# Kernel tuning notes

Measured on AMD Instinct MI355X. Metric: run time of the kernel, lower is better.

## Reference

```python
import jax, jax.numpy as jnp
import numpy as np

N = 8192
TOKEN_DIM = 384
K = 16
D_IN = 2 * (TOKEN_DIM + 3)  # 774


def setup_inputs() -> dict:
    key = jax.random.key(0)
    k1, k2, k3, k4, k5, k6 = jax.random.split(key, 6)
    xyz = jax.random.normal(k1, (N, 3), dtype=jnp.float32)
    feat = jax.random.normal(k2, (N, TOKEN_DIM), dtype=jnp.float32)
    W1 = jax.random.normal(k3, (D_IN, TOKEN_DIM), dtype=jnp.float32) / np.sqrt(D_IN)
    b1 = jax.random.normal(k4, (TOKEN_DIM,), dtype=jnp.float32) * 0.01
    W2 = jax.random.normal(k5, (TOKEN_DIM, 3), dtype=jnp.float32) / np.sqrt(TOKEN_DIM)
    b2 = jax.random.normal(k6, (3,), dtype=jnp.float32) * 0.01
    return {"xyz": xyz, "feat": feat, "W1": W1, "b1": b1, "W2": W2, "b2": b2}


def _knn_idx(xyz, k):
    # pairwise squared distances [N, N]; loop=False -> exclude self via +inf diag
    sq = jnp.sum(xyz * xyz, axis=-1)
    d2 = sq[:, None] + sq[None, :] - 2.0 * (xyz @ xyz.T)
    n = xyz.shape[0]
    d2 = jnp.where(jnp.eye(n, dtype=bool), jnp.inf, d2)
    _, idx = jax.lax.top_k(-d2, k)  # idx[i] = k nearest neighbors (sources) of target i
    return idx


def reference(xyz, feat, W1, b1, W2, b2):
    idx = _knn_idx(xyz, K)                      # [N, K] int32
    x = jnp.concatenate([feat, xyz], axis=-1)   # [N, D] with D = token_dim + 3
    x_j = x[idx]                                # [N, K, D] gathered neighbor feats
    x_i = x[:, None, :]                         # [N, 1, D]
    # EdgeConv message: nn(cat([x_i, x_j - x_i]))
    e = jnp.concatenate([jnp.broadcast_to(x_i, x_j.shape), x_j - x_i], axis=-1)  # [N, K, 2D]
    h = jax.nn.relu(jnp.einsum('nkd,df->nkf', e, W1) + b1)   # [N, K, token_dim]
    m = jnp.einsum('nkf,fo->nko', h, W2) + b2                # [N, K, 3]
    agg = jnp.max(m, axis=1)                                 # max aggregation over neighbors
    return xyz + agg
```

## Files before the change

### kernel.cpp

```cpp
#include <hip/hip_runtime.h>
#include <hip/hip_bf16.h>


#define N 8192
#define TD 384
#define KNN 16
#define DX 387
#define KP 416
#define NF 768
#define INFF __builtin_inff()

typedef __attribute__((ext_vector_type(8))) short short8;
typedef __attribute__((ext_vector_type(4))) float f32x4;
typedef __attribute__((ext_vector_type(2))) float f32x2;


__device__ __forceinline__ f32x2 pk_mul(f32x2 a, f32x2 b) {
    f32x2 r; asm("v_pk_mul_f32 %0, %1, %2" : "=v"(r) : "v"(a), "v"(b)); return r;
}
__device__ __forceinline__ f32x2 pk_add(f32x2 a, f32x2 b) {
    f32x2 r; asm("v_pk_add_f32 %0, %1, %2" : "=v"(r) : "v"(a), "v"(b)); return r;
}
__device__ __forceinline__ f32x2 pk_sub(f32x2 a, f32x2 b) {
    f32x2 r; asm("v_pk_add_f32 %0, %1, %2 neg_lo:[0,1] neg_hi:[0,1]" : "=v"(r) : "v"(a), "v"(b)); return r;
}
__device__ __forceinline__ f32x2 pk_fma(f32x2 a, f32x2 b, f32x2 c) {
    f32x2 r; asm("v_pk_fma_f32 %0, %1, %2, %3" : "=v"(r) : "v"(a), "v"(b), "v"(c)); return r;
}

__device__ __forceinline__ void dist4(f32x2 qx, f32x2 qy, f32x2 qz, f32x2 qw,
                                      f32x2 x01, f32x2 x23, f32x2 y01, f32x2 y23,
                                      f32x2 z01, f32x2 z23, f32x2 s01, f32x2 s23,
                                      f32x2& d01, f32x2& d23) {
    f32x2 dot01 = pk_fma(qz, z01, pk_fma(qy, y01, pk_mul(qx, x01)));
    f32x2 dot23 = pk_fma(qz, z23, pk_fma(qy, y23, pk_mul(qx, x23)));
    d01 = pk_sub(pk_add(qw, s01), pk_add(dot01, dot01));
    d23 = pk_sub(pk_add(qw, s23), pk_add(dot23, dot23));
}

__device__ __forceinline__ int xbin(float x) {
    int b = (int)((x + 4.0f) * 32.0f);
    return b < 0 ? 0 : (b > 255 ? 255 : b);
}


__global__ void __launch_bounds__(128) prep_all(const float* __restrict__ feat,
                                                const float* __restrict__ xyz,
                                                const float* __restrict__ W1,
                                                __hip_bfloat16* __restrict__ Xb,
                                                __hip_bfloat16* __restrict__ Wpt,
                                                int* __restrict__ cut) {
    int b = blockIdx.x;
    int t = threadIdx.x;
    if (b < N) {
        if (t < 96) {
            float4 f = reinterpret_cast<const float4*>(feat + (size_t)b*TD)[t];
            __hip_bfloat16 h[4] = {__float2bfloat16(f.x), __float2bfloat16(f.y),
                                   __float2bfloat16(f.z), __float2bfloat16(f.w)};
            *reinterpret_cast<ulonglong1*>(Xb + b*KP + t*4) = *reinterpret_cast<ulonglong1*>(h);
        } else if (t == 96) {
            for (int d = TD; d < KP; ++d) {
                float v = (d < DX) ? xyz[b*3 + (d - TD)] : 0.f;
                Xb[b*KP + d] = __float2bfloat16(v);
            }
        }
    } else if (b < N + NF) {
        int f = b - N;
        for (int k = t; k < KP; k += 128) {
            float v = 0.f;
            if (k < DX) {
                if (f < TD) v = W1[k*TD + f] - W1[(DX+k)*TD + f];
                else        v = W1[(DX+k)*TD + (f - TD)];
            }
            Wpt[f*KP + k] = __float2bfloat16(v);
        }
    } else {
        cut[t] = 0;
        cut[t + 128] = 0;
    }
}


__global__ void __launch_bounds__(256) assign_kernel(const float* __restrict__ xyz,
                                                     int* __restrict__ cut,
                                                     int* __restrict__ tlo,
                                                     int* __restrict__ thi,
                                                     float* __restrict__ stile) {
    __shared__ int hcnt[256];
    __shared__ int base[256];
    __shared__ int stlo[32], sthi[32];
    const int t = threadIdx.x;

    hcnt[t] = 0;
    if (t < 32) { stlo[t] = 255; sthi[t] = 0; }
    __syncthreads();

    #pragma unroll
    for (int c = 0; c < 32; ++c) {
        atomicAdd(&hcnt[xbin(xyz[(t + c*256)*3])], 1);
    }
    __syncthreads();

    const int v = hcnt[t];
    base[t] = v;
    __syncthreads();
    for (int off = 1; off < 256; off <<= 1) {
        int add = (t >= off) ? base[t - off] : 0;
        __syncthreads();
        base[t] += add;
        __syncthreads();
    }
    const int end = base[t], start = end - v;
    __syncthreads();
    base[t] = start;
    __syncthreads();

    if (blockIdx.x == 0) {
        if (v > 0) {
            for (int x = start >> 8; x <= (end - 1) >> 8; ++x) {
                atomicMin(&stlo[x], t);
                atomicMax(&sthi[x], t);
            }
        }
        __syncthreads();
        if (t < 32) { tlo[t] = stlo[t]; thi[t] = sthi[t]; }
    }

    const int i = blockIdx.x * 256 + t;
    float x = xyz[i*3+0], y = xyz[i*3+1], z = xyz[i*3+2];
    int bin = xbin(x);
    int pos = base[bin] + atomicAdd(&cut[bin], 1);
    float sq = __fadd_rn(__fadd_rn(__fmul_rn(x,x), __fmul_rn(y,y)), __fmul_rn(z,z));
    float* tp = stile + (pos >> 8) * 1280 + (pos & 255);
    tp[0] = x; tp[256] = y; tp[512] = z; tp[768] = sq;
    reinterpret_cast<int*>(tp)[1024] = i;
}


__device__ __forceinline__ float rdlane_f(float v, int src) {
    return __uint_as_float(__builtin_amdgcn_readlane(__float_as_uint(v), src));
}
__device__ __forceinline__ unsigned udmap(float x) {
    unsigned u = __float_as_uint(x);
    return ((int)u < 0) ? ~u : (u | 0x80000000u);
}


__global__ void __launch_bounds__(256, 8) knn_kernel(const float* __restrict__ stile,
                                                     const int* __restrict__ tlo,
                                                     const int* __restrict__ thi,
                                                     int* __restrict__ knn) {
    __shared__ unsigned sbuf[4][128][2];
    const int lane = threadIdx.x & 63;
    const int wv   = threadIdx.x >> 6;
    const int s    = blockIdx.x * 4 + wv;
    const int tq   = s >> 8;
    const int sl   = (s & 255) >> 2;
    const int slot = s & 3;

    const float* qp = stile + tq*1280 + (s & 255);
    const float qx = qp[0], qy = qp[256], qz = qp[512], qw = qp[768];
    const int   qi = reinterpret_cast<const int*>(qp)[1024];
    const f32x2 qx2 = {qx,qx}, qy2 = {qy,qy}, qz2 = {qz,qz}, qw2 = {qw,qw};

    const float* lbase = stile + lane*4;
    const bool is_self_lane = (lane == sl);

    float mn = INFF;
    int lo = tq - 2; if (lo < 0) lo = 0; if (lo > 27) lo = 27;
    #pragma unroll
    for (int tt = 0; tt < 5; ++tt) {
        const int t = lo + tt;
        const float* tp = lbase + t*1280;
        float4 X = *(const float4*)(tp);
        float4 Y = *(const float4*)(tp + 256);
        float4 Z = *(const float4*)(tp + 512);
        float4 S = *(const float4*)(tp + 768);
        f32x2 x01 = {X.x,X.y}, x23 = {X.z,X.w};
        f32x2 y01 = {Y.x,Y.y}, y23 = {Y.z,Y.w};
        f32x2 z01 = {Z.x,Z.y}, z23 = {Z.z,Z.w};
        f32x2 s01 = {S.x,S.y}, s23 = {S.z,S.w};
        f32x2 d01, d23;
        dist4(qx2, qy2, qz2, qw2, x01, x23, y01, y23, z01, z23, s01, s23, d01, d23);
        if ((t == tq) && is_self_lane) {
            if      (slot == 0) d01[0] = INFF;
            else if (slot == 1) d01[1] = INFF;
            else if (slot == 2) d23[0] = INFF;
            else                d23[1] = INFF;
        }
        mn = fminf(mn, fminf(fminf(d01[0], d01[1]), fminf(d23[0], d23[1])));
    }

    float T;
    {
        unsigned ub = udmap(mn);
        unsigned long long alive = ~0ull;
        int need = KNN;
        #pragma unroll
        for (int b = 31; b >= 0; --b) {
            unsigned long long ones  = __ballot(((ub >> b) & 1u) != 0u);
            unsigned long long zeros = alive & ~ones;
            int cz = (int)__popcll(zeros);
            bool tz = (cz >= need);
            alive = tz ? zeros : (alive & ones);
            need  = tz ? need : (need - cz);
        }
        T = fmaxf(rdlane_f(mn, (int)__ffsll(alive) - 1), 0.f);
    }

    unsigned mask;
    {
        const int ti = lane & 31;
        const int bl = tlo[ti], bh = thi[ti];
        const float xlo = (bl == 0)   ? -1e30f : (bl * 0.03125f - 4.0f);
        const float xhi = (bh == 255) ?  1e30f : ((bh + 1) * 0.03125f - 4.0f);
        float gap = fmaxf(0.f, fmaxf(xlo - qx, qx - xhi));
        bool gate = (gap * gap <= T + 1e-3f);
        mask = (unsigned)__ballot(gate && (lane < 32));
    }

    int cnt = 0;
    const unsigned long long ltm = (1ull << lane) - 1;

    auto push = [&](float dv, int idx) {
        bool pred = (dv <= T);
        unsigned long long bal = __ballot(pred);
        if (bal) {
            int posn = cnt + (int)__popcll(bal & ltm);
            if (pred && posn < 128) {
                sbuf[wv][posn][0] = udmap(dv);
                sbuf[wv][posn][1] = (unsigned)idx;
            }
            cnt += (int)__popcll(bal);
        }
    };

    while (mask) {
        const int t = (int)__ffs(mask) - 1;
        mask &= mask - 1;
        const float* tp = lbase + t*1280;
        float4 X = *(const float4*)(tp);
        float4 Y = *(const float4*)(tp + 256);
        float4 Z = *(const float4*)(tp + 512);
        float4 S = *(const float4*)(tp + 768);
        int4   I = *(const int4*)(tp + 1024);
        f32x2 x01 = {X.x,X.y}, x23 = {X.z,X.w};
        f32x2 y01 = {Y.x,Y.y}, y23 = {Y.z,Y.w};
        f32x2 z01 = {Z.x,Z.y}, z23 = {Z.z,Z.w};
        f32x2 s01 = {S.x,S.y}, s23 = {S.z,S.w};
        f32x2 d01, d23;
        dist4(qx2, qy2, qz2, qw2, x01, x23, y01, y23, z01, z23, s01, s23, d01, d23);
        if ((t == tq) && is_self_lane) {
            if      (slot == 0) d01[0] = INFF;
            else if (slot == 1) d01[1] = INFF;
            else if (slot == 2) d23[0] = INFF;
            else                d23[1] = INFF;
        }
        float tmin = fminf(fminf(d01[0], d01[1]), fminf(d23[0], d23[1]));
        if (__ballot(tmin <= T)) {
            push(d01[0], I.x);
            push(d01[1], I.y);
            push(d23[0], I.z);
            push(d23[1], I.w);
        }
    }

    asm volatile("s_waitcnt lgkmcnt(0)" ::: "memory");
    const int M = (cnt > 128) ? 128 : cnt;
    unsigned ud1 = 0xFFFFFFFFu, id1 = 0xFFFFFFFFu;
    unsigned ud2 = 0xFFFFFFFFu, id2 = 0xFFFFFFFFu;
    if (lane < M)      { ud1 = sbuf[wv][lane][0];      id1 = sbuf[wv][lane][1]; }
    if (lane + 64 < M) { ud2 = sbuf[wv][lane + 64][0]; id2 = sbuf[wv][lane + 64][1]; }

    unsigned long long alive1 = __ballot(lane < M);
    unsigned long long alive2 = __ballot(lane + 64 < M);
    int need = KNN;
    #pragma unroll
    for (int b = 31; b >= 0; --b) {
        unsigned long long on1 = __ballot(((ud1 >> b) & 1u) != 0u);
        unsigned long long on2 = __ballot(((ud2 >> b) & 1u) != 0u);
        unsigned long long z1 = alive1 & ~on1;
        unsigned long long z2 = alive2 & ~on2;
        int cz = (int)__popcll(z1) + (int)__popcll(z2);
        bool tz = (cz >= need);
        alive1 = tz ? z1 : (alive1 & on1);
        alive2 = tz ? z2 : (alive2 & on2);
        need   = tz ? need : (need - cz);
    }
    unsigned v16;
    if (alive1) v16 = (unsigned)__builtin_amdgcn_readlane((int)ud1, (int)__ffsll(alive1) - 1);
    else        v16 = (unsigned)__builtin_amdgcn_readlane((int)ud2, (int)__ffsll(alive2) - 1);

    const int nt = (int)__popcll(alive1) + (int)__popcll(alive2);
    const bool all_ties = (nt <= need);
    unsigned vidx = 0xFFFFFFFFu;
    if (!all_ties) {
        unsigned long long a1 = alive1, a2 = alive2;
        int nd = need;
        for (int b = 31; b >= 0; --b) {
            unsigned long long on1 = __ballot(((id1 >> b) & 1u) != 0u);
            unsigned long long on2 = __ballot(((id2 >> b) & 1u) != 0u);
            unsigned long long z1 = a1 & ~on1;
            unsigned long long z2 = a2 & ~on2;
            int cz = (int)__popcll(z1) + (int)__popcll(z2);
            bool tz = (cz >= nd);
            a1 = tz ? z1 : (a1 & on1);
            a2 = tz ? z2 : (a2 & on2);
            nd = tz ? nd : (nd - cz);
        }
        if (a1) vidx = (unsigned)__builtin_amdgcn_readlane((int)id1, (int)__ffsll(a1) - 1);
        else    vidx = (unsigned)__builtin_amdgcn_readlane((int)id2, (int)__ffsll(a2) - 1);
    }

    bool sel1 = (lane < M)      && ((ud1 < v16) || ((ud1 == v16) && (all_ties || (id1 <= vidx))));
    bool sel2 = (lane + 64 < M) && ((ud2 < v16) || ((ud2 == v16) && (all_ties || (id2 <= vidx))));
    unsigned long long bs1 = __ballot(sel1);
    if (sel1) knn[qi*KNN + (int)__popcll(bs1 & ltm)] = (int)id1;
    const int c1 = (int)__popcll(bs1);
    unsigned long long bs2 = __ballot(sel2);
    if (sel2) knn[qi*KNN + c1 + (int)__popcll(bs2 & ltm)] = (int)id2;
}


__global__ void __launch_bounds__(64) gemm_kernel(const __hip_bfloat16* __restrict__ Xb,
                                                  const __hip_bfloat16* __restrict__ Wpt,
                                                  const float* __restrict__ b1,
                                                  __hip_bfloat16* __restrict__ Ub,
                                                  __hip_bfloat16* __restrict__ Vb) {
    const int lane = threadIdx.x;
    const int i0   = blockIdx.x * 64;
    const int f0   = blockIdx.y * 64;
    const int lm   = lane & 15;
    const int lk   = (lane >> 4) * 8;

    f32x4 acc[4][4];
    #pragma unroll
    for (int r = 0; r < 4; ++r)
        #pragma unroll
        for (int c = 0; c < 4; ++c)
            acc[r][c] = (f32x4){0.f, 0.f, 0.f, 0.f};

    const __hip_bfloat16* xbase = Xb  + (size_t)(i0 + lm) * KP + lk;
    const __hip_bfloat16* wbase = Wpt + (size_t)(f0 + lm) * KP + lk;

    #pragma unroll
    for (int kk = 0; kk < 13; ++kk) {
        short8 a[4], b[4];
        #pragma unroll
        for (int r = 0; r < 4; ++r)
            a[r] = *reinterpret_cast<const short8*>(xbase + (size_t)r*16*KP + kk*32);
        #pragma unroll
        for (int c = 0; c < 4; ++c)
            b[c] = *reinterpret_cast<const short8*>(wbase + (size_t)c*16*KP + kk*32);
        #pragma unroll
        for (int r = 0; r < 4; ++r)
            #pragma unroll
            for (int c = 0; c < 4; ++c)
                acc[r][c] = __builtin_amdgcn_mfma_f32_16x16x32_bf16(a[r], b[c], acc[r][c], 0, 0, 0);
    }

    const bool isU = (f0 < TD);
    __hip_bfloat16* outb = isU ? (Ub + f0) : (Vb + (f0 - TD));
    float bias[4] = {0.f, 0.f, 0.f, 0.f};
    if (isU) {
        #pragma unroll
        for (int c = 0; c < 4; ++c) bias[c] = b1[f0 + c*16 + lm];
    }
    const int crow = (lane >> 4) * 4;
    #pragma unroll
    for (int r = 0; r < 4; ++r)
        #pragma unroll
        for (int c = 0; c < 4; ++c)
            #pragma unroll
            for (int q = 0; q < 4; ++q)
                outb[(size_t)(i0 + r*16 + crow + q) * TD + c*16 + lm] =
                    __float2bfloat16(acc[r][c][q] + bias[c]);
}


__device__ __forceinline__ float bflo(unsigned w) { return __uint_as_float(w << 16); }
__device__ __forceinline__ float bfhi(unsigned w) { return __uint_as_float(w & 0xFFFF0000u); }

template<int CTRL>
__device__ __forceinline__ float dppf(float v) {
    return __uint_as_float((unsigned)__builtin_amdgcn_update_dpp(
        0, (int)__float_as_uint(v), CTRL, 0xF, 0xF, true));
}

__global__ void __launch_bounds__(256) final_kernel(const __hip_bfloat16* __restrict__ Ub,
                                                    const __hip_bfloat16* __restrict__ Vb,
                                                    const int* __restrict__ knn,
                                                    const float* __restrict__ xyz,
                                                    const float* __restrict__ W2,
                                                    const float* __restrict__ b2,
                                                    float* __restrict__ out) {
    const int lane = threadIdx.x & 63;
    const int wv   = threadIdx.x >> 6;
    const int i    = blockIdx.x * 4 + wv;
    const int d0   = lane * 6;

    int jreg = knn[i*KNN + (lane & 15)];

    float u[6], w2l[6][3];
    {
        const unsigned* rowU = reinterpret_cast<const unsigned*>(Ub + (size_t)i * TD) + lane*3;
        unsigned a0 = rowU[0], a1 = rowU[1], a2 = rowU[2];
        u[0] = bflo(a0); u[1] = bfhi(a0);
        u[2] = bflo(a1); u[3] = bfhi(a1);
        u[4] = bflo(a2); u[5] = bfhi(a2);
    }
    #pragma unroll
    for (int t = 0; t < 6; ++t)
        #pragma unroll
        for (int c = 0; c < 3; ++c) w2l[t][c] = W2[(d0 + t)*3 + c];

    const unsigned* vbase = reinterpret_cast<const unsigned*>(Vb);
    const int voff = lane * 3;

    float pk0[16], pk1[16], pk2[16];
    unsigned va[2][4][3];

    #pragma unroll
    for (int t = 0; t < 4; ++t) {
        int j = __builtin_amdgcn_readlane(jreg, t);
        const unsigned* rv = vbase + (size_t)j * 192 + voff;
        va[0][t][0] = rv[0]; va[0][t][1] = rv[1]; va[0][t][2] = rv[2];
    }
    __builtin_amdgcn_sched_barrier(0);

    #pragma unroll
    for (int b = 0; b < 4; ++b) {
        if (b < 3) {
            #pragma unroll
            for (int t = 0; t < 4; ++t) {
                int j = __builtin_amdgcn_readlane(jreg, (b+1)*4 + t);
                const unsigned* rv = vbase + (size_t)j * 192 + voff;
                va[(b+1)&1][t][0] = rv[0];
                va[(b+1)&1][t][1] = rv[1];
                va[(b+1)&1][t][2] = rv[2];
            }
            __builtin_amdgcn_sched_barrier(0);
        }
        #pragma unroll
        for (int t = 0; t < 4; ++t) {
            const int kk = b*4 + t;
            unsigned a0 = va[b&1][t][0], a1 = va[b&1][t][1], a2 = va[b&1][t][2];
            float v0 = bflo(a0), v1 = bfhi(a0);
            float v2 = bflo(a1), v3 = bfhi(a1);
            float v4 = bflo(a2), v5 = bfhi(a2);
            float h0 = fmaxf(u[0] + v0, 0.f), h1 = fmaxf(u[1] + v1, 0.f);
            float h2 = fmaxf(u[2] + v2, 0.f), h3 = fmaxf(u[3] + v3, 0.f);
            float h4 = fmaxf(u[4] + v4, 0.f), h5 = fmaxf(u[5] + v5, 0.f);
            float s0 = 0.f, s1 = 0.f, s2 = 0.f;
            s0 = fmaf(h0, w2l[0][0], s0); s1 = fmaf(h0, w2l[0][1], s1); s2 = fmaf(h0, w2l[0][2], s2);
            s0 = fmaf(h1, w2l[1][0], s0); s1 = fmaf(h1, w2l[1][1], s1); s2 = fmaf(h1, w2l[1][2], s2);
            s0 = fmaf(h2, w2l[2][0], s0); s1 = fmaf(h2, w2l[2][1], s1); s2 = fmaf(h2, w2l[2][2], s2);
            s0 = fmaf(h3, w2l[3][0], s0); s1 = fmaf(h3, w2l[3][1], s1); s2 = fmaf(h3, w2l[3][2], s2);
            s0 = fmaf(h4, w2l[4][0], s0); s1 = fmaf(h4, w2l[4][1], s1); s2 = fmaf(h4, w2l[4][2], s2);
            s0 = fmaf(h5, w2l[5][0], s0); s1 = fmaf(h5, w2l[5][1], s1); s2 = fmaf(h5, w2l[5][2], s2);
            pk0[kk] = s0; pk1[kk] = s1; pk2[kk] = s2;
        }
    }

    #pragma unroll
    for (int kk = 0; kk < 16; ++kk) {
        float r0 = pk0[kk], r1 = pk1[kk], r2 = pk2[kk];
        r0 += dppf<0x121>(r0); r1 += dppf<0x121>(r1); r2 += dppf<0x121>(r2);
        r0 += dppf<0x122>(r0); r1 += dppf<0x122>(r1); r2 += dppf<0x122>(r2);
        r0 += dppf<0x124>(r0); r1 += dppf<0x124>(r1); r2 += dppf<0x124>(r2);
        r0 += dppf<0x128>(r0); r1 += dppf<0x128>(r1); r2 += dppf<0x128>(r2);
        r0 += __shfl_xor(r0, 16); r1 += __shfl_xor(r1, 16); r2 += __shfl_xor(r2, 16);
        r0 += __shfl_xor(r0, 32); r1 += __shfl_xor(r1, 32); r2 += __shfl_xor(r2, 32);
        pk0[kk] = r0; pk1[kk] = r1; pk2[kk] = r2;
    }
    float mx0 = pk0[0], mx1 = pk1[0], mx2 = pk2[0];
    #pragma unroll
    for (int kk = 1; kk < 16; ++kk) {
        mx0 = fmaxf(mx0, pk0[kk]);
        mx1 = fmaxf(mx1, pk1[kk]);
        mx2 = fmaxf(mx2, pk2[kk]);
    }

    if (lane == 0) {
        out[i*3+0] = xyz[i*3+0] + mx0 + b2[0];
        out[i*3+1] = xyz[i*3+1] + mx1 + b2[1];
        out[i*3+2] = xyz[i*3+2] + mx2 + b2[2];
    }
}


extern "C" void kernel_launch(void* const* d_in, const int* in_sizes, int n_in,
                              void* d_out, int out_size, void* d_ws, size_t ws_size,
                              hipStream_t stream) {
    const float* xyz  = (const float*)d_in[0];
    const float* feat = (const float*)d_in[1];
    const float* W1   = (const float*)d_in[2];
    const float* b1   = (const float*)d_in[3];
    const float* W2   = (const float*)d_in[4];
    const float* b2   = (const float*)d_in[5];
    float* out = (float*)d_out;

    char* ws = (char*)d_ws;
    int*            knn   = (int*)(ws + 0);
    float*          stile = (float*)(ws + 524288);
    __hip_bfloat16* Xb    = (__hip_bfloat16*)(ws + 688128);
    __hip_bfloat16* Wpt   = (__hip_bfloat16*)(ws + 7503872);
    __hip_bfloat16* Ub    = (__hip_bfloat16*)(ws + 8142848);
    __hip_bfloat16* Vb    = (__hip_bfloat16*)(ws + 14434304);
    int*            cut   = (int*)(ws + 20725760);
    int*            thi   = (int*)(ws + 20726784);
    int*            tlo   = (int*)(ws + 20726912);

    prep_all     <<<dim3(N + NF + 1),  dim3(128), 0, stream>>>(feat, xyz, W1, Xb, Wpt, cut);
    assign_kernel<<<dim3(N/256),       dim3(256), 0, stream>>>(xyz, cut, tlo, thi, stile);
    knn_kernel   <<<dim3(N/4),         dim3(256), 0, stream>>>(stile, tlo, thi, knn);
    gemm_kernel  <<<dim3(N/64, NF/64), dim3(64),  0, stream>>>(Xb, Wpt, b1, Ub, Vb);
    final_kernel <<<dim3(N/4),         dim3(256), 0, stream>>>(Ub, Vb, knn, xyz, W2, b2, out);
}
```

Before: 85.96 us.

## Cache first-pass KNN distances in LDS and add single-wave fast select path

The KNN kernel now stores the distances computed for the first five tiles in shared memory and reuses them in the candidate-collection pass instead of reloading coordinates and recomputing. A specialised one-register selection path runs when there are at most 64 candidates, and the prep kernel now writes the xyz/pad columns in parallel across threads instead of in a one-thread loop. The extra LDS (20KB per block) lowers the occupancy hint from 8 to 6 waves, trading occupancy for less recompute and fewer global loads.

```diff
diff --git a/kernel.cpp b/kernel.cpp
--- a/kernel.cpp
+++ b/kernel.cpp
@@ -58,11 +58,10 @@
             __hip_bfloat16 h[4] = {__float2bfloat16(f.x), __float2bfloat16(f.y),
                                    __float2bfloat16(f.z), __float2bfloat16(f.w)};
             *reinterpret_cast<ulonglong1*>(Xb + b*KP + t*4) = *reinterpret_cast<ulonglong1*>(h);
-        } else if (t == 96) {
-            for (int d = TD; d < KP; ++d) {
-                float v = (d < DX) ? xyz[b*3 + (d - TD)] : 0.f;
-                Xb[b*KP + d] = __float2bfloat16(v);
-            }
+        } else {
+            int d = TD + (t - 96);
+            float v = (d < DX) ? xyz[b*3 + (d - TD)] : 0.f;
+            Xb[b*KP + d] = __float2bfloat16(v);
         }
     } else if (b < N + NF) {
         int f = b - N;
@@ -146,10 +145,11 @@
 }
 
 
-__global__ void __launch_bounds__(256, 8) knn_kernel(const float* __restrict__ stile,
+__global__ void __launch_bounds__(256, 6) knn_kernel(const float* __restrict__ stile,
                                                      const int* __restrict__ tlo,
                                                      const int* __restrict__ thi,
                                                      int* __restrict__ knn) {
+    __shared__ float    dcache[4][5][256];
     __shared__ unsigned sbuf[4][128][2];
     const int lane = threadIdx.x & 63;
     const int wv   = threadIdx.x >> 6;
@@ -188,7 +188,9 @@
             else if (slot == 2) d23[0] = INFF;
             else                d23[1] = INFF;
         }
-        mn = fminf(mn, fminf(fminf(d01[0], d01[1]), fminf(d23[0], d23[1])));
+        f32x4 dd = {d01[0], d01[1], d23[0], d23[1]};
+        *reinterpret_cast<f32x4*>(&dcache[wv][tt][lane*4]) = dd;
+        mn = fminf(mn, fminf(fminf(dd[0], dd[1]), fminf(dd[2], dd[3])));
     }
 
     float T;
@@ -235,9 +237,21 @@
         }
     };
 
-    while (mask) {
-        const int t = (int)__ffs(mask) - 1;
-        mask &= mask - 1;
+    #pragma unroll
+    for (int tt = 0; tt < 5; ++tt) {
+        const int t = lo + tt;
+        if (!((mask >> t) & 1u)) continue;
+        f32x4 dd = *reinterpret_cast<const f32x4*>(&dcache[wv][tt][lane*4]);
+        int4 I = *(const int4*)(lbase + t*1280 + 1024);
+        push(dd[0], I.x);
+        push(dd[1], I.y);
+        push(dd[2], I.z);
+        push(dd[3], I.w);
+    }
+    unsigned rest = mask & ~(0x1Fu << lo);
+    while (rest) {
+        const int t = (int)__ffs(rest) - 1;
+        rest &= rest - 1;
         const float* tp = lbase + t*1280;
         float4 X = *(const float4*)(tp);
         float4 Y = *(const float4*)(tp + 256);
@@ -250,12 +264,6 @@
         f32x2 s01 = {S.x,S.y}, s23 = {S.z,S.w};
         f32x2 d01, d23;
         dist4(qx2, qy2, qz2, qw2, x01, x23, y01, y23, z01, z23, s01, s23, d01, d23);
-        if ((t == tq) && is_self_lane) {
-            if      (slot == 0) d01[0] = INFF;
-            else if (slot == 1) d01[1] = INFF;
-            else if (slot == 2) d23[0] = INFF;
-            else                d23[1] = INFF;
-        }
         float tmin = fminf(fminf(d01[0], d01[1]), fminf(d23[0], d23[1]));
         if (__ballot(tmin <= T)) {
             push(d01[0], I.x);
@@ -267,58 +275,94 @@
 
     asm volatile("s_waitcnt lgkmcnt(0)" ::: "memory");
     const int M = (cnt > 128) ? 128 : cnt;
-    unsigned ud1 = 0xFFFFFFFFu, id1 = 0xFFFFFFFFu;
-    unsigned ud2 = 0xFFFFFFFFu, id2 = 0xFFFFFFFFu;
-    if (lane < M)      { ud1 = sbuf[wv][lane][0];      id1 = sbuf[wv][lane][1]; }
-    if (lane + 64 < M) { ud2 = sbuf[wv][lane + 64][0]; id2 = sbuf[wv][lane + 64][1]; }
-
-    unsigned long long alive1 = __ballot(lane < M);
-    unsigned long long alive2 = __ballot(lane + 64 < M);
-    int need = KNN;
-    #pragma unroll
-    for (int b = 31; b >= 0; --b) {
-        unsigned long long on1 = __ballot(((ud1 >> b) & 1u) != 0u);
-        unsigned long long on2 = __ballot(((ud2 >> b) & 1u) != 0u);
-        unsigned long long z1 = alive1 & ~on1;
-        unsigned long long z2 = alive2 & ~on2;
-        int cz = (int)__popcll(z1) + (int)__popcll(z2);
-        bool tz = (cz >= need);
-        alive1 = tz ? z1 : (alive1 & on1);
-        alive2 = tz ? z2 : (alive2 & on2);
-        need   = tz ? need : (need - cz);
-    }
-    unsigned v16;
-    if (alive1) v16 = (unsigned)__builtin_amdgcn_readlane((int)ud1, (int)__ffsll(alive1) - 1);
-    else        v16 = (unsigned)__builtin_amdgcn_readlane((int)ud2, (int)__ffsll(alive2) - 1);
-
-    const int nt = (int)__popcll(alive1) + (int)__popcll(alive2);
-    const bool all_ties = (nt <= need);
-    unsigned vidx = 0xFFFFFFFFu;
-    if (!all_ties) {
-        unsigned long long a1 = alive1, a2 = alive2;
-        int nd = need;
+
+    if (M <= 64) {
+        unsigned ud1 = 0xFFFFFFFFu, id1 = 0xFFFFFFFFu;
+        if (lane < M) { ud1 = sbuf[wv][lane][0]; id1 = sbuf[wv][lane][1]; }
+        unsigned long long alive = __ballot(lane < M);
+        int need = KNN;
+        #pragma unroll
         for (int b = 31; b >= 0; --b) {
-            unsigned long long on1 = __ballot(((id1 >> b) & 1u) != 0u);
-            unsigned long long on2 = __ballot(((id2 >> b) & 1u) != 0u);
-            unsigned long long z1 = a1 & ~on1;
-            unsigned long long z2 = a2 & ~on2;
+            unsigned long long on = __ballot(((ud1 >> b) & 1u) != 0u);
+            unsigned long long z  = alive & ~on;
+            int cz = (int)__popcll(z);
+            bool tz = (cz >= need);
+            alive = tz ? z : (alive & on);
+            need  = tz ? need : (need - cz);
+        }
+        unsigned v16 = (unsigned)__builtin_amdgcn_readlane((int)ud1, (int)__ffsll(alive) - 1);
+        const bool all_ties = ((int)__popcll(alive) <= need);
+        unsigned vidx = 0xFFFFFFFFu;
+        if (!all_ties) {
+            unsigned long long a = alive;
+            int nd = need;
+            for (int b = 31; b >= 0; --b) {
+                unsigned long long on = __ballot(((id1 >> b) & 1u) != 0u);
+                unsigned long long z  = a & ~on;
+                int cz = (int)__popcll(z);
+                bool tz = (cz >= nd);
+                a  = tz ? z : (a & on);
+                nd = tz ? nd : (nd - cz);
+            }
+            vidx = (unsigned)__builtin_amdgcn_readlane((int)id1, (int)__ffsll(a) - 1);
+        }
+        bool sel = (lane < M) && ((ud1 < v16) || ((ud1 == v16) && (all_ties || (id1 <= vidx))));
+        unsigned long long bs = __ballot(sel);
+        if (sel) knn[qi*KNN + (int)__popcll(bs & ltm)] = (int)id1;
+    } else {
+        unsigned ud1 = 0xFFFFFFFFu, id1 = 0xFFFFFFFFu;
+        unsigned ud2 = 0xFFFFFFFFu, id2 = 0xFFFFFFFFu;
+        if (lane < M)      { ud1 = sbuf[wv][lane][0];      id1 = sbuf[wv][lane][1]; }
+        if (lane + 64 < M) { ud2 = sbuf[wv][lane + 64][0]; id2 = sbuf[wv][lane + 64][1]; }
+
+        unsigned long long alive1 = __ballot(lane < M);
+        unsigned long long alive2 = __ballot(lane + 64 < M);
+        int need = KNN;
+        #pragma unroll
+        for (int b = 31; b >= 0; --b) {
+            unsigned long long on1 = __ballot(((ud1 >> b) & 1u) != 0u);
+            unsigned long long on2 = __ballot(((ud2 >> b) & 1u) != 0u);
+            unsigned long long z1 = alive1 & ~on1;
+            unsigned long long z2 = alive2 & ~on2;
             int cz = (int)__popcll(z1) + (int)__popcll(z2);
-            bool tz = (cz >= nd);
-            a1 = tz ? z1 : (a1 & on1);
-            a2 = tz ? z2 : (a2 & on2);
-            nd = tz ? nd : (nd - cz);
-        }
-        if (a1) vidx = (unsigned)__builtin_amdgcn_readlane((int)id1, (int)__ffsll(a1) - 1);
-        else    vidx = (unsigned)__builtin_amdgcn_readlane((int)id2, (int)__ffsll(a2) - 1);
-    }
-
-    bool sel1 = (lane < M)      && ((ud1 < v16) || ((ud1 == v16) && (all_ties || (id1 <= vidx))));
-    bool sel2 = (lane + 64 < M) && ((ud2 < v16) || ((ud2 == v16) && (all_ties || (id2 <= vidx))));
-    unsigned long long bs1 = __ballot(sel1);
-    if (sel1) knn[qi*KNN + (int)__popcll(bs1 & ltm)] = (int)id1;
-    const int c1 = (int)__popcll(bs1);
-    unsigned long long bs2 = __ballot(sel2);
-    if (sel2) knn[qi*KNN + c1 + (int)__popcll(bs2 & ltm)] = (int)id2;
+            bool tz = (cz >= need);
+            alive1 = tz ? z1 : (alive1 & on1);
+            alive2 = tz ? z2 : (alive2 & on2);
+            need   = tz ? need : (need - cz);
+        }
+        unsigned v16;
+        if (alive1) v16 = (unsigned)__builtin_amdgcn_readlane((int)ud1, (int)__ffsll(alive1) - 1);
+        else        v16 = (unsigned)__builtin_amdgcn_readlane((int)ud2, (int)__ffsll(alive2) - 1);
+
+        const int nt = (int)__popcll(alive1) + (int)__popcll(alive2);
+        const bool all_ties = (nt <= need);
+        unsigned vidx = 0xFFFFFFFFu;
+        if (!all_ties) {
+            unsigned long long a1 = alive1, a2 = alive2;
+            int nd = need;
+            for (int b = 31; b >= 0; --b) {
+                unsigned long long on1 = __ballot(((id1 >> b) & 1u) != 0u);
+                unsigned long long on2 = __ballot(((id2 >> b) & 1u) != 0u);
+                unsigned long long z1 = a1 & ~on1;
+                unsigned long long z2 = a2 & ~on2;
+                int cz = (int)__popcll(z1) + (int)__popcll(z2);
+                bool tz = (cz >= nd);
+                a1 = tz ? z1 : (a1 & on1);
+                a2 = tz ? z2 : (a2 & on2);
+                nd = tz ? nd : (nd - cz);
+            }
+            if (a1) vidx = (unsigned)__builtin_amdgcn_readlane((int)id1, (int)__ffsll(a1) - 1);
+            else    vidx = (unsigned)__builtin_amdgcn_readlane((int)id2, (int)__ffsll(a2) - 1);
+        }
+
+        bool sel1 = (lane < M)      && ((ud1 < v16) || ((ud1 == v16) && (all_ties || (id1 <= vidx))));
+        bool sel2 = (lane + 64 < M) && ((ud2 < v16) || ((ud2 == v16) && (all_ties || (id2 <= vidx))));
+        unsigned long long bs1 = __ballot(sel1);
+        if (sel1) knn[qi*KNN + (int)__popcll(bs1 & ltm)] = (int)id1;
+        const int c1 = (int)__popcll(bs1);
+        unsigned long long bs2 = __ballot(sel2);
+        if (sel2) knn[qi*KNN + c1 + (int)__popcll(bs2 & ltm)] = (int)id2;
+    }
 }
 
 
```

Result: faster. 82.45 us (-4.1%).
